# Optimization experiments

Measured on AMD Instinct MI355X. Metric: run time of the kernel, lower is better.

## Reference

```python
import jax, jax.numpy as jnp
from jax import lax
import numpy as np

DN = ('NHWC', 'HWIO', 'NHWC')


def extract_patches(x, k, stride):
    # tf.image.extract_patches with sizes [1,k,k,1], strides [1,s,s,1], SAME padding.
    # Output depth ordering matches TF: (ki, kj, channel).
    B, H, W, C = x.shape
    oh = -(-H // stride)
    ow = -(-W // stride)
    ph = max((oh - 1) * stride + k - H, 0)
    pw = max((ow - 1) * stride + k - W, 0)
    xp = jnp.pad(x, ((0, 0), (ph // 2, ph - ph // 2), (pw // 2, pw - pw // 2), (0, 0)))
    cols = [xp[:, i:i + stride * (oh - 1) + 1:stride, j:j + stride * (ow - 1) + 1:stride, :]
            for i in range(k) for j in range(k)]
    return jnp.stack(cols, axis=3).reshape(B, oh, ow, k * k * C)


def contextual_attention(x, mask_s, rate=2, fuse_k=3, softmax_scale=10.0):
    B, H, W, C = x.shape
    k = rate * 2 - 1  # 3
    # raw (full-resolution) patches used as deconv filters: [B,k,k,C,L]
    raw = extract_patches(x, k, rate)
    h, w = raw.shape[1], raw.shape[2]
    L = h * w
    raw_f = raw.reshape(B, L, k, k, C).transpose(0, 2, 3, 4, 1)
    # downsample src/ref by rate (extract_patches with size 1 == strided slice)
    src = x[:, ::rate, ::rate, :]  # [B,h,w,C]
    feats = extract_patches(src, k, 1).reshape(B, L, k, k, C).transpose(0, 2, 3, 4, 1)  # [B,k,k,C,L]
    # NOTE: source normalizes by sum of squares over axes (0,1,2) = (batch,kh,kw) -> [C,L], no sqrt
    denom = jnp.maximum(jnp.sum(feats * feats, axis=(0, 1, 2)), 1e-8)
    ref_feat = feats / denom
    # mask: maxpool 16/16 then 3/1, then invert
    m = lax.reduce_window(mask_s, -jnp.inf, lax.max, (1, 16, 16, 1), (1, 16, 16, 1), 'SAME')
    m = lax.reduce_window(m, -jnp.inf, lax.max, (1, 3, 3, 1), (1, 1, 1, 1), 'SAME')
    mm = 1.0 - m  # [B,h,w,1]
    # per-sample correlation: conv src_b with its own normalized patch bank
    corr = lambda s, f: lax.conv_general_dilated(s[None], f, (1, 1), 'SAME', dimension_numbers=DN)[0]
    y = jax.vmap(corr)(src, ref_feat)  # [B,h,w,L]
    # fuse: diagonal (identity) 3x3 convs over the (query, key) score plane, both orderings
    fuse_w = jnp.eye(fuse_k, dtype=x.dtype).reshape(fuse_k, fuse_k, 1, 1)
    yi = y.reshape(B, h * w, L, 1)
    yi = lax.conv_general_dilated(yi, fuse_w, (1, 1), 'SAME', dimension_numbers=DN)
    yi = yi.reshape(B, h, w, h, w).transpose(0, 2, 1, 4, 3).reshape(B, h * w, L, 1)
    yi = lax.conv_general_dilated(yi, fuse_w, (1, 1), 'SAME', dimension_numbers=DN)
    y = yi.reshape(B, w, h, w, h).transpose(0, 2, 1, 4, 3).reshape(B, h, w, L)
    # masked softmax over reference patches
    y = jax.nn.softmax(y * mm * softmax_scale, axis=-1) * mm
    # per-sample transposed conv (paste raw patches), matching tf.nn.conv2d_transpose SAME stride=rate
    pt = max((h - 1) * rate + k - H, 0)
    pl = max((w - 1) * rate + k - W, 0)
    pad_h = (k - 1 - pt // 2, k - 1 - (pt - pt // 2))
    pad_w = (k - 1 - pl // 2, k - 1 - (pl - pl // 2))

    def deconv(y_b, f_b):
        wg = jnp.flip(f_b, axis=(0, 1)).swapaxes(2, 3)  # [k,k,L,C]
        return lax.conv_general_dilated(y_b[None], wg, (1, 1), (pad_h, pad_w),
                                        lhs_dilation=(rate, rate), dimension_numbers=DN)[0]

    y_up = jax.vmap(deconv)(y, raw_f)  # [B,H,W,C]
    return y_up, y


def gated_conv(x, w, b, dw, pw, db):
    # gen_conv_gated_ds: Conv2D -> ELU gated by SeparableConv2D -> channel softmax
    x1 = jax.nn.elu(lax.conv_general_dilated(x, w, (1, 1), 'SAME', dimension_numbers=DN) + b)
    x2 = lax.conv_general_dilated(x, dw, (1, 1), 'SAME', feature_group_count=x.shape[-1],
                                  dimension_numbers=DN)
    x2 = lax.conv_general_dilated(x2, pw, (1, 1), 'SAME', dimension_numbers=DN) + db
    return x1 * jax.nn.softmax(x2, axis=-1)


def setup_inputs():
    key = jax.random.key(0)
    ks = jax.random.split(key, 8)
    B, H, W, C, dim = 8, 64, 64, 128, 128
    s = 0.05
    x = jax.random.normal(ks[0], (B, H, W, C), jnp.float32)
    mask_s = jnp.zeros((B, 16 * H // 2, 16 * W // 2, 1), jnp.float32)
    mask_s = mask_s.at[:, 128:384, 128:384, :].set(1.0)
    return {
        'x': x,
        'mask_s': mask_s,
        'w1': jax.random.normal(ks[1], (3, 3, C, dim), jnp.float32) * s,
        'b1': jnp.zeros((dim,), jnp.float32),
        'dw1': jax.random.normal(ks[2], (3, 3, 1, C), jnp.float32) * s,
        'pw1': jax.random.normal(ks[3], (1, 1, C, dim), jnp.float32) * s,
        'db1': jnp.zeros((dim,), jnp.float32),
        'w2': jax.random.normal(ks[4], (3, 3, dim + C, dim), jnp.float32) * s,
        'b2': jnp.zeros((dim,), jnp.float32),
        'dw2': jax.random.normal(ks[5], (3, 3, 1, dim + C), jnp.float32) * s,
        'pw2': jax.random.normal(ks[6], (1, 1, dim + C, dim), jnp.float32) * s,
        'db2': jnp.zeros((dim,), jnp.float32),
    }


def reference(x, mask_s, w1, b1, dw1, pw1, db1, w2, b2, dw2, pw2, db2):
    y_up, corres = contextual_attention(x, mask_s)
    a = gated_conv(y_up, w1, b1, dw1, pw1, db1)
    a = jnp.concatenate([a, x], axis=3)
    a = gated_conv(a, w2, b2, dw2, pw2, db2)
    return a, corres
```

## Files before the change

### kernel.cpp

```cpp
#include <hip/hip_runtime.h>
#include <hip/hip_bf16.h>


#define BOFF_SP      0
#define BOFF_INVD    4734976
#define BOFF_SP16    5259264
#define BOFF_BF16    7626752
#define BOFF_T       0
#define BOFF_BP16    0
#define BOFF_YP16    18874368
#define BOFF_YUP     37748736
#define BOFF_SM      0
#define BOFF_P316    16777216
#define BOFF_A1      25698304
#define BOFF_X16     42475520
#define BOFF_WT1     69238784
#define BOFF_WT2     69828608
#define BOFF_PW1     71008256
#define BOFF_PW2     71041024
#define BOFF_M0      71106560
#define BOFF_MM      71139328

typedef float f32x4 __attribute__((ext_vector_type(4)));
typedef _Float16 f16x8 __attribute__((ext_vector_type(8)));

__global__ __launch_bounds__(256) void k_mask_pool(const float* __restrict__ mask, float* __restrict__ m0) {
    int blk = blockIdx.x;
    int b = blk >> 10, pq = blk & 1023, p = pq >> 5, q = pq & 31;
    int t = threadIdx.x, dy = t >> 4, dx = t & 15;
    float v = mask[((size_t)(b * 512 + p * 16 + dy)) * 512 + q * 16 + dx];
#pragma unroll
    for (int o = 32; o; o >>= 1) v = fmaxf(v, __shfl_xor(v, o));
    __shared__ float s[4];
    if ((t & 63) == 0) s[t >> 6] = v;
    __syncthreads();
    if (t == 0) m0[blk] = fmaxf(fmaxf(s[0], s[1]), fmaxf(s[2], s[3]));
}

__global__ void k_mask_dilate(const float* __restrict__ m0, float* __restrict__ mm) {
    int idx = blockIdx.x * 256 + threadIdx.x;
    if (idx >= 8192) return;
    int b = idx >> 10, pq = idx & 1023, p = pq >> 5, q = pq & 31;
    float v = -1e30f;
    for (int di = -1; di <= 1; ++di)
        for (int dj = -1; dj <= 1; ++dj) {
            int pp = p + di, qq = q + dj;
            if (pp >= 0 && pp < 32 && qq >= 0 && qq < 32)
                v = fmaxf(v, m0[(b << 10) + pp * 32 + qq]);
        }
    mm[idx] = 1.0f - v;
}

__global__ void k_srcpad(const float* __restrict__ x, float* __restrict__ sp) {
    int idx = blockIdx.x * 256 + threadIdx.x;
    if (idx >= 8 * 34 * 34 * 128) return;
    int c = idx & 127;
    int r = idx >> 7;
    int xx = r % 34; r /= 34;
    int yy = r % 34; int b = r / 34;
    float v = 0.f;
    if (yy >= 1 && yy <= 32 && xx >= 1 && xx <= 32)
        v = x[(((size_t)(b * 64 + (yy - 1) * 2)) * 64 + (xx - 1) * 2) * 128 + c];
    sp[idx] = v;
}

__global__ void k_sp16(const float* __restrict__ sp, _Float16* __restrict__ o) {
    int idx = blockIdx.x * 256 + threadIdx.x;
    if (idx >= 147968) return;
    const float* s = sp + (size_t)idx * 8;
    float4 v0 = *reinterpret_cast<const float4*>(s);
    float4 v1 = *reinterpret_cast<const float4*>(s + 4);
    f16x8 h;
    h[0] = (_Float16)v0.x; h[1] = (_Float16)v0.y; h[2] = (_Float16)v0.z; h[3] = (_Float16)v0.w;
    h[4] = (_Float16)v1.x; h[5] = (_Float16)v1.y; h[6] = (_Float16)v1.z; h[7] = (_Float16)v1.w;
    *reinterpret_cast<f16x8*>(o + (size_t)idx * 8) = h;
}

__global__ void k_invd(const float* __restrict__ sp, float* __restrict__ invd) {
    int idx = blockIdx.x * 256 + threadIdx.x;
    if (idx >= 1024 * 128) return;
    int c = idx & 127, l = idx >> 7, lh = l >> 5, lw = l & 31;
    float s = 0.f;
    for (int b = 0; b < 8; ++b)
#pragma unroll
        for (int i = 0; i < 3; ++i)
#pragma unroll
            for (int j = 0; j < 3; ++j) {
                float v = sp[(((size_t)(b * 34 + lh + i)) * 34 + (lw + j)) * 128 + c];
                s += v * v;
            }
    invd[idx] = 1.0f / fmaxf(s, 1e-8f);
}

__global__ void k_corr_B16(const float* __restrict__ sp, const float* __restrict__ invd,
                           _Float16* __restrict__ bf) {
    int idx = blockIdx.x * 256 + threadIdx.x;
    if (idx >= 1179648) return;
    int c8 = idx & 15; int rest = idx >> 4;
    int ij = rest % 9; int rest2 = rest / 9;
    int l = rest2 & 1023, b = rest2 >> 10;
    int lh = l >> 5, lw = l & 31;
    int i = (ij >= 6) ? 2 : (ij >= 3 ? 1 : 0);
    int j = ij - 3 * i;
    int c0 = c8 * 8;
    const float* s = sp + (((size_t)(b * 34 + lh + i)) * 34 + (lw + j)) * 128 + c0;
    const float* dv = invd + l * 128 + c0;
    f16x8 h;
#pragma unroll
    for (int u = 0; u < 8; ++u) h[u] = (_Float16)(s[u] * dv[u]);
    size_t off = ((size_t)(b * 1024 + l)) * 1152 + ij * 128 + c0;
    *reinterpret_cast<f16x8*>(bf + off) = h;
}

__global__ void k_deconv_B16(const float* __restrict__ x, _Float16* __restrict__ bp) {
    int idx = blockIdx.x * 256 + threadIdx.x;
    if (idx >= 1179648) return;
    int l8 = idx & 127; int rest = idx >> 7;
    int c = rest & 127; int rest2 = rest >> 7;
    int ij = rest2 % 9; int b = rest2 / 9;
    int ip = (ij >= 6) ? 2 : (ij >= 3 ? 1 : 0);
    int jp = ij - 3 * ip;
    int l0 = l8 * 8;
    int lh = l0 >> 5, lw0 = l0 & 31;
    int rr = 2 * lh + ip;
    f16x8 h;
#pragma unroll
    for (int u = 0; u < 8; ++u) {
        int ss = 2 * (lw0 + u) + jp;
        float v = (rr < 64 && ss < 64) ? x[(((size_t)(b * 64 + rr)) * 64 + ss) * 128 + c] : 0.f;
        h[u] = (_Float16)v;
    }
    size_t off = (((size_t)(b * 9 + ij)) * 128 + c) * 1024 + l0;
    *reinterpret_cast<f16x8*>(bp + off) = h;
}

__global__ __launch_bounds__(512) void k_corr_mfma(const _Float16* __restrict__ sp16,
                                                   const _Float16* __restrict__ bf,
                                                   float* __restrict__ outy) {
    const int bid = blockIdx.x;
    const int xcd = bid & 7, slot = bid >> 3;
    const int tm = slot & 7, pg = slot >> 3;
    const int panel = pg * 8 + xcd;
    const int b = panel >> 4, tn = panel & 15;
    __shared__ _Float16 Aa[128][40];
    __shared__ _Float16 Ab[128][40];
    const int tid = threadIdx.x;
    const int w = tid >> 6, lane = tid & 63, m = lane & 15, g = lane >> 4;
    const int rh = w & 1, cg = w >> 1;
    f32x4 acc[4];
#pragma unroll
    for (int mf = 0; mf < 4; ++mf) acc[mf] = f32x4{0.f, 0.f, 0.f, 0.f};
    const int srow = tid >> 2, scc = (tid & 3) * 8;
    const int pq = tm * 128 + srow, p = pq >> 5, q = pq & 31;
    const int col0 = tn * 64 + cg * 16 + m;
    const size_t boff = ((size_t)b * 1024 + col0) * 1152 + g * 8;

    auto aoff = [&](int kt) -> size_t {
        int ij = kt >> 7;
        int i = (ij >= 6) ? 2 : (ij >= 3 ? 1 : 0);
        int j = ij - 3 * i;
        int c0 = (kt & 127) + scc;
        return (((size_t)(b * 34 + p + i)) * 34 + (q + j)) * 128 + c0;
    };
    f16x8 ara = *reinterpret_cast<const f16x8*>(sp16 + aoff(0));
    f16x8 arb = *reinterpret_cast<const f16x8*>(sp16 + aoff(32));
    f16x8 nba = *reinterpret_cast<const f16x8*>(bf + boff);
    f16x8 nbb = *reinterpret_cast<const f16x8*>(bf + boff + 32);

    for (int kt = 0; kt < 1152; kt += 64) {
        __syncthreads();
        *reinterpret_cast<f16x8*>(&Aa[srow][scc]) = ara;
        *reinterpret_cast<f16x8*>(&Ab[srow][scc]) = arb;
        __syncthreads();
        const int ktn = (kt + 64 < 1152) ? kt + 64 : kt;
        f16x8 cba = nba, cbb = nbb;
        ara = *reinterpret_cast<const f16x8*>(sp16 + aoff(ktn));
        arb = *reinterpret_cast<const f16x8*>(sp16 + aoff(ktn + 32));
        nba = *reinterpret_cast<const f16x8*>(bf + boff + ktn);
        nbb = *reinterpret_cast<const f16x8*>(bf + boff + ktn + 32);

        f16x8 av;
#pragma unroll
        for (int mf = 0; mf < 4; ++mf) {
            av = *reinterpret_cast<const f16x8*>(&Aa[rh * 64 + mf * 16 + m][g * 8]);
            acc[mf] = __builtin_amdgcn_mfma_f32_16x16x32_f16(av, cba, acc[mf], 0, 0, 0);
            av = *reinterpret_cast<const f16x8*>(&Ab[rh * 64 + mf * 16 + m][g * 8]);
            acc[mf] = __builtin_amdgcn_mfma_f32_16x16x32_f16(av, cbb, acc[mf], 0, 0, 0);
        }
    }
#pragma unroll
    for (int mf = 0; mf < 4; ++mf) {
        int row = tm * 128 + rh * 64 + mf * 16 + g * 4;
#pragma unroll
        for (int r = 0; r < 4; ++r)
            outy[((size_t)b << 20) + (size_t)(row + r) * 1024 + col0] = acc[mf][r];
    }
}

__global__ __launch_bounds__(512) void k_deconv_mfma(const _Float16* __restrict__ yp16,
                                                     const _Float16* __restrict__ bp,
                                                     float* __restrict__ yup) {
    const int bid = blockIdx.x;
    const int xcd = bid & 7, slot = bid >> 3;
    const int tm = slot & 7, pg = slot >> 3;
    const int panel = pg * 8 + xcd;
    const int b = panel / 9, tn = panel % 9;
    __shared__ _Float16 Aa[128][40];
    __shared__ _Float16 Ab[128][40];
    const int tid = threadIdx.x;
    const int w = tid >> 6, lane = tid & 63, m = lane & 15, g = lane >> 4;
    const int rh = w & 1, cg = w >> 1;
    f32x4 acc[4][2];
#pragma unroll
    for (int mf = 0; mf < 4; ++mf)
#pragma unroll
        for (int nn = 0; nn < 2; ++nn) acc[mf][nn] = f32x4{0.f, 0.f, 0.f, 0.f};
    const int srow = tid >> 2, scc = (tid & 3) * 8;
    const int c0 = cg * 32 + m;
    const _Float16* abase = yp16 + ((size_t)b << 20) + (size_t)(tm * 128 + srow) * 1024 + scc;
    const size_t boff0 = (((size_t)(b * 9 + tn)) * 128 + c0) * 1024 + g * 8;
    const size_t boff1 = (((size_t)(b * 9 + tn)) * 128 + c0 + 16) * 1024 + g * 8;

    f16x8 ara = *reinterpret_cast<const f16x8*>(abase);
    f16x8 arb = *reinterpret_cast<const f16x8*>(abase + 32);
    f16x8 nb0a = *reinterpret_cast<const f16x8*>(bp + boff0);
    f16x8 nb0b = *reinterpret_cast<const f16x8*>(bp + boff0 + 32);
    f16x8 nb1a = *reinterpret_cast<const f16x8*>(bp + boff1);
    f16x8 nb1b = *reinterpret_cast<const f16x8*>(bp + boff1 + 32);

    for (int kt = 0; kt < 1024; kt += 64) {
        __syncthreads();
        *reinterpret_cast<f16x8*>(&Aa[srow][scc]) = ara;
        *reinterpret_cast<f16x8*>(&Ab[srow][scc]) = arb;
        __syncthreads();
        const int ktn = (kt + 64 < 1024) ? kt + 64 : kt;
        f16x8 cb0a = nb0a, cb0b = nb0b, cb1a = nb1a, cb1b = nb1b;
        ara = *reinterpret_cast<const f16x8*>(abase + ktn);
        arb = *reinterpret_cast<const f16x8*>(abase + ktn + 32);
        nb0a = *reinterpret_cast<const f16x8*>(bp + boff0 + ktn);
        nb0b = *reinterpret_cast<const f16x8*>(bp + boff0 + ktn + 32);
        nb1a = *reinterpret_cast<const f16x8*>(bp + boff1 + ktn);
        nb1b = *reinterpret_cast<const f16x8*>(bp + boff1 + ktn + 32);

        f16x8 av;
#pragma unroll
        for (int mf = 0; mf < 4; ++mf) {
            av = *reinterpret_cast<const f16x8*>(&Aa[rh * 64 + mf * 16 + m][g * 8]);
            acc[mf][0] = __builtin_amdgcn_mfma_f32_16x16x32_f16(av, cb0a, acc[mf][0], 0, 0, 0);
            acc[mf][1] = __builtin_amdgcn_mfma_f32_16x16x32_f16(av, cb1a, acc[mf][1], 0, 0, 0);
            av = *reinterpret_cast<const f16x8*>(&Ab[rh * 64 + mf * 16 + m][g * 8]);
            acc[mf][0] = __builtin_amdgcn_mfma_f32_16x16x32_f16(av, cb0b, acc[mf][0], 0, 0, 0);
            acc[mf][1] = __builtin_amdgcn_mfma_f32_16x16x32_f16(av, cb1b, acc[mf][1], 0, 0, 0);
        }
    }
    const int ip = (tn >= 6) ? 2 : (tn >= 3 ? 1 : 0);
    const int jp = tn - 3 * ip;
#pragma unroll
    for (int mf = 0; mf < 4; ++mf) {
        int uvb = tm * 128 + rh * 64 + mf * 16 + g * 4;
#pragma unroll
        for (int nn = 0; nn < 2; ++nn) {
            int c = c0 + nn * 16;
#pragma unroll
            for (int r = 0; r < 4; ++r) {
                int uv = uvb + r;
                int uu = uv >> 5, vv = uv & 31;
                int P = 2 * uu + ip, Q = 2 * vv + jp;
                if (P < 64 && Q < 64)
                    atomicAdd(&yup[(((size_t)(b * 64 + P)) * 64 + Q) * 128 + c], acc[mf][nn][r]);
            }
        }
    }
}

__global__ void k_fuse1(const float* __restrict__ in, float* __restrict__ out) {
    size_t idx = (size_t)blockIdx.x * 256 + threadIdx.x;
    if (idx >= (size_t)8 * 1024 * 1024) return;
    int t = (int)(idx & 1023);
    int s = (int)((idx >> 10) & 1023);
    int b = (int)(idx >> 20);
    const float* base = in + ((size_t)b << 20);
    float v = base[(size_t)s * 1024 + t];
    if (s > 0 && t > 0) v += base[(size_t)(s - 1) * 1024 + (t - 1)];
    if (s < 1023 && t < 1023) v += base[(size_t)(s + 1) * 1024 + (t + 1)];
    out[idx] = v;
}

__global__ void k_fuse2(const float* __restrict__ in, float* __restrict__ out) {
    size_t idx = (size_t)blockIdx.x * 256 + threadIdx.x;
    if (idx >= (size_t)8 * 1024 * 1024) return;
    int t = (int)(idx & 1023);
    int s = (int)((idx >> 10) & 1023);
    int b = (int)(idx >> 20);
    int m0 = ((s & 31) << 5) + (s >> 5);
    int n0 = ((t & 31) << 5) + (t >> 5);
    const float* base = in + ((size_t)b << 20);
    float v = 0.f;
#pragma unroll
    for (int d = -1; d <= 1; ++d) {
        int m = m0 + d, n = n0 + d;
        if (m >= 0 && m < 1024 && n >= 0 && n < 1024)
            v += base[(size_t)(((m & 31) << 5) + (m >> 5)) * 1024 + (((n & 31) << 5) + (n >> 5))];
    }
    out[idx] = v;
}

__global__ __launch_bounds__(256) void k_softmax1024(const float* __restrict__ yv,
                                                     const float* __restrict__ mm,
                                                     float* __restrict__ outc,
                                                     _Float16* __restrict__ yp16) {
    int row = blockIdx.x;
    const float* base = yv + (size_t)row * 1024;
    float mmv = mm[row];
    int t = threadIdx.x;
    float vals[4];
    float mx = -1e30f;
#pragma unroll
    for (int i = 0; i < 4; ++i) {
        vals[i] = base[t + i * 256] * mmv * 10.0f;
        mx = fmaxf(mx, vals[i]);
    }
#pragma unroll
    for (int o = 32; o; o >>= 1) mx = fmaxf(mx, __shfl_xor(mx, o));
    __shared__ float red[8];
    if ((t & 63) == 0) red[t >> 6] = mx;
    __syncthreads();
    mx = fmaxf(fmaxf(red[0], red[1]), fmaxf(red[2], red[3]));
    float s = 0.f;
#pragma unroll
    for (int i = 0; i < 4; ++i) {
        vals[i] = expf(vals[i] - mx);
        s += vals[i];
    }
#pragma unroll
    for (int o = 32; o; o >>= 1) s += __shfl_xor(s, o);
    if ((t & 63) == 0) red[4 + (t >> 6)] = s;
    __syncthreads();
    s = red[4] + red[5] + red[6] + red[7];
    float inv = mmv / s;
#pragma unroll
    for (int i = 0; i < 4; ++i) {
        float pv = vals[i] * inv;
        outc[(size_t)row * 1024 + t + i * 256] = pv;
        yp16[(size_t)row * 1024 + t + i * 256] = (_Float16)pv;
    }
}

__global__ __launch_bounds__(256) void k_pad16(const float* __restrict__ in,
                                               _Float16* __restrict__ o) {
    int idx = blockIdx.x * 256 + threadIdx.x;
    int c8 = idx & 15;
    int r = idx >> 4;
    int pc = r % 66; r /= 66;
    int pr = r % 66; int b = r / 66;
    f16x8 h;
    if (pr >= 1 && pr <= 64 && pc >= 1 && pc <= 64) {
        const float* s = in + (((size_t)(b * 64 + pr - 1)) * 64 + (pc - 1)) * 128 + c8 * 8;
        float4 v0 = *reinterpret_cast<const float4*>(s);
        float4 v1 = *reinterpret_cast<const float4*>(s + 4);
        h[0] = (_Float16)v0.x; h[1] = (_Float16)v0.y; h[2] = (_Float16)v0.z; h[3] = (_Float16)v0.w;
        h[4] = (_Float16)v1.x; h[5] = (_Float16)v1.y; h[6] = (_Float16)v1.z; h[7] = (_Float16)v1.w;
    } else {
#pragma unroll
        for (int u = 0; u < 8; ++u) h[u] = (_Float16)0.f;
    }
    *reinterpret_cast<f16x8*>(o + (size_t)idx * 8) = h;
}

__global__ void k_wt16(const float* __restrict__ w, _Float16* __restrict__ o, int CI) {
    int idx = blockIdx.x * 256 + threadIdx.x;
    if (idx >= 9 * CI * 128) return;
    int ci = idx % CI; int rest = idx / CI;
    int co = rest & 127; int ij = rest >> 7;
    o[idx] = (_Float16)w[((size_t)ij * CI + ci) * 128 + co];
}

__global__ void k_pw16(const float* __restrict__ pw, _Float16* __restrict__ out, int CI) {
    int idx = blockIdx.x * 256 + threadIdx.x;
    if (idx >= CI * 128) return;
    int co = idx & 127, ci = idx >> 7;
    out[(size_t)co * CI + ci] = (_Float16)pw[idx];
}

template <int CI>
__global__ __launch_bounds__(256, 2) void k_dwpw_mfma(const _Float16* __restrict__ in0,
                                                      const _Float16* __restrict__ in1,
                                                      const float* __restrict__ dwW,
                                                      const _Float16* __restrict__ pwt,
                                                      const float* __restrict__ db,
                                                      float* __restrict__ smout) {
    const int bid = blockIdx.x;
    const int swz = (bid & 7) * 64 + (bid >> 3);
    const int b = swz >> 6, P = swz & 63;
    const int t = threadIdx.x;
    const int w = t >> 6, lane = t & 63, m = lane & 15, g = lane >> 4;
    __shared__ _Float16 Adw[64 * CI];
    __shared__ float red[2][4][64];
    char* ab = (char*)Adw;
    const int px = lane;
    const int cb = w * (CI / 4);
    float dwacc[CI / 4];
#pragma unroll
    for (int u = 0; u < CI / 4; ++u) dwacc[u] = 0.f;
#pragma unroll
    for (int i = 0; i < 3; ++i) {
#pragma unroll
        for (int j = 0; j < 3; ++j) {
            const int ij = i * 3 + j;
#pragma unroll
            for (int c8 = 0; c8 < CI / 32; ++c8) {
                const int c = cb + c8 * 8;
                const _Float16* ph = (CI == 256 && c >= 128) ? in1 : in0;
                const int cc = (CI == 256 && c >= 128) ? (c - 128) : c;
                size_t off = (((size_t)b * 66 + P + i) * 66 + px + j) * 128 + cc;
                f16x8 vh = *reinterpret_cast<const f16x8*>(ph + off);
#pragma unroll
                for (int u = 0; u < 8; ++u)
                    dwacc[c8 * 8 + u] = fmaf((float)vh[u], dwW[ij * CI + c + u], dwacc[c8 * 8 + u]);
            }
        }
    }
#pragma unroll
    for (int c8 = 0; c8 < CI / 32; ++c8) {
        f16x8 hv;
#pragma unroll
        for (int u = 0; u < 8; ++u) hv[u] = (_Float16)dwacc[c8 * 8 + u];
        int byte = px * (CI * 2) + (cb + c8 * 8) * 2;
        int sz = byte ^ ((px & 7) << 4);
        *reinterpret_cast<f16x8*>(ab + sz) = hv;
    }
    __syncthreads();
    f32x4 acc[4][2];
#pragma unroll
    for (int mt = 0; mt < 4; ++mt)
#pragma unroll
        for (int nn = 0; nn < 2; ++nn) acc[mt][nn] = f32x4{0.f, 0.f, 0.f, 0.f};
    const int co0 = w * 32 + m;
#pragma unroll
    for (int kc = 0; kc < CI / 32; ++kc) {
        f16x8 av[4];
#pragma unroll
        for (int mt = 0; mt < 4; ++mt) {
            int prow = mt * 16 + m;
            int byte = prow * (CI * 2) + (kc * 32 + g * 8) * 2;
            int sz = byte ^ ((prow & 7) << 4);
            av[mt] = *reinterpret_cast<const f16x8*>(ab + sz);
        }
#pragma unroll
        for (int nn = 0; nn < 2; ++nn) {
            f16x8 bv = *reinterpret_cast<const f16x8*>(pwt + (size_t)(co0 + nn * 16) * CI + kc * 32 + g * 8);
#pragma unroll
            for (int mt = 0; mt < 4; ++mt)
                acc[mt][nn] = __builtin_amdgcn_mfma_f32_16x16x32_f16(av[mt], bv, acc[mt][nn], 0, 0, 0);
        }
    }
    float db0 = db[co0], db1 = db[co0 + 16];
    float mx[4][4];
#pragma unroll
    for (int mt = 0; mt < 4; ++mt)
#pragma unroll
        for (int r = 0; r < 4; ++r) {
            acc[mt][0][r] += db0;
            acc[mt][1][r] += db1;
            float v = fmaxf(acc[mt][0][r], acc[mt][1][r]);
#pragma unroll
            for (int o = 1; o <= 8; o <<= 1) v = fmaxf(v, __shfl_xor(v, o));
            mx[mt][r] = v;
        }
    if (m == 0) {
#pragma unroll
        for (int mt = 0; mt < 4; ++mt)
#pragma unroll
            for (int r = 0; r < 4; ++r) red[0][w][mt * 16 + g * 4 + r] = mx[mt][r];
    }
    __syncthreads();
    float sume[4][4];
#pragma unroll
    for (int mt = 0; mt < 4; ++mt)
#pragma unroll
        for (int r = 0; r < 4; ++r) {
            int p = mt * 16 + g * 4 + r;
            float M = fmaxf(fmaxf(red[0][0][p], red[0][1][p]), fmaxf(red[0][2][p], red[0][3][p]));
            acc[mt][0][r] = expf(acc[mt][0][r] - M);
            acc[mt][1][r] = expf(acc[mt][1][r] - M);
            float s = acc[mt][0][r] + acc[mt][1][r];
#pragma unroll
            for (int o = 1; o <= 8; o <<= 1) s += __shfl_xor(s, o);
            sume[mt][r] = s;
        }
    if (m == 0) {
#pragma unroll
        for (int mt = 0; mt < 4; ++mt)
#pragma unroll
            for (int r = 0; r < 4; ++r) red[1][w][mt * 16 + g * 4 + r] = sume[mt][r];
    }
    __syncthreads();
#pragma unroll
    for (int mt = 0; mt < 4; ++mt)
#pragma unroll
        for (int r = 0; r < 4; ++r) {
            int p = mt * 16 + g * 4 + r;
            float S = red[1][0][p] + red[1][1][p] + red[1][2][p] + red[1][3][p];
            float inv = 1.0f / S;
            size_t pix = ((size_t)b * 64 + P) * 64 + p;
            smout[pix * 128 + co0] = acc[mt][0][r] * inv;
            smout[pix * 128 + co0 + 16] = acc[mt][1][r] * inv;
        }
}

template <int CI>
__global__ __launch_bounds__(256, 4) void k_conv_lds(const _Float16* __restrict__ in0,
                                                     const _Float16* __restrict__ in1,
                                                     const _Float16* __restrict__ wt,
                                                     const float* __restrict__ bias,
                                                     const float* __restrict__ sm,
                                                     float* __restrict__ out) {
    const int bid = blockIdx.x;
    const int idx = (bid & 7) * 128 + (bid >> 3);
    const int row = idx >> 1, cohalf = idx & 1;
    const int b = row >> 6, P = row & 63;
    const int tid = threadIdx.x;
    const int w = tid >> 6, lane = tid & 63;
    const int m = lane & 15, g = lane >> 4;
    __shared__ _Float16 S[66 * 128];
    char* sb = (char*)S;
    f32x4 acc[4];
#pragma unroll
    for (int mt = 0; mt < 4; ++mt) acc[mt] = f32x4{0.f, 0.f, 0.f, 0.f};
    const int cow = cohalf * 64 + w * 16 + m;

#pragma unroll
    for (int half = 0; half < CI / 128; ++half) {
        const _Float16* ih = (half == 0) ? in0 : in1;
        const size_t rbase0 = ((size_t)b * 66 + P) * 66 * 128;
#pragma unroll
        for (int i = 0; i < 3; ++i) {
            __syncthreads();
            const size_t rsrc = rbase0 + (size_t)i * 66 * 128;
#pragma unroll
            for (int e0 = 0; e0 < 1056; e0 += 256) {
                int e = e0 + tid;
                if (e < 1056) {
                    int px = e >> 4, c8 = e & 15;
                    int lin = px * 256 + c8 * 16;
                    int sz = lin ^ ((px & 7) << 4);
                    size_t so = rsrc + (size_t)px * 128 + c8 * 8;
                    *reinterpret_cast<f16x8*>(sb + sz) = *reinterpret_cast<const f16x8*>(ih + so);
                }
            }
            __syncthreads();
#pragma unroll
            for (int j = 0; j < 3; ++j) {
                const int ij = i * 3 + j;
                const _Float16* wp = wt + ((size_t)ij * 128 + cow) * CI + half * 128 + g * 8;
#pragma unroll
                for (int ci0 = 0; ci0 < 128; ci0 += 32) {
                    f16x8 bv = *reinterpret_cast<const f16x8*>(wp + ci0);
                    f16x8 av[4];
#pragma unroll
                    for (int mt = 0; mt < 4; ++mt) {
                        int px = mt * 16 + m + j;
                        int lin = px * 256 + ci0 * 2 + g * 16;
                        int sz = lin ^ ((px & 7) << 4);
                        av[mt] = *reinterpret_cast<const f16x8*>(sb + sz);
                    }
#pragma unroll
                    for (int mt = 0; mt < 4; ++mt)
                        acc[mt] = __builtin_amdgcn_mfma_f32_16x16x32_f16(av[mt], bv, acc[mt], 0, 0, 0);
                }
            }
        }
    }
    const float bb = bias[cow];
#pragma unroll
    for (int mt = 0; mt < 4; ++mt) {
#pragma unroll
        for (int r = 0; r < 4; ++r) {
            int Q = mt * 16 + g * 4 + r;
            size_t pix = ((size_t)b * 64 + P) * 64 + Q;
            float z = acc[mt][r] + bb;
            z = z > 0.f ? z : expm1f(z);
            out[pix * 128 + cow] = z * sm[pix * 128 + cow];
        }
    }
}

extern "C" void kernel_launch(void* const* d_in, const int* in_sizes, int n_in,
                              void* d_out, int out_size, void* d_ws, size_t ws_size,
                              hipStream_t stream) {
    const float* x    = (const float*)d_in[0];
    const float* mask = (const float*)d_in[1];
    const float* w1   = (const float*)d_in[2];
    const float* b1   = (const float*)d_in[3];
    const float* dw1  = (const float*)d_in[4];
    const float* pw1  = (const float*)d_in[5];
    const float* db1  = (const float*)d_in[6];
    const float* w2   = (const float*)d_in[7];
    const float* b2   = (const float*)d_in[8];
    const float* dw2  = (const float*)d_in[9];
    const float* pw2  = (const float*)d_in[10];
    const float* db2  = (const float*)d_in[11];

    float* out_a = (float*)d_out;
    float* out_c = out_a + 4194304;

    char* wsb = (char*)d_ws;
    float* sp      = (float*)(wsb + BOFF_SP);
    float* invd    = (float*)(wsb + BOFF_INVD);
    _Float16* sp16 = (_Float16*)(wsb + BOFF_SP16);
    _Float16* bf16b = (_Float16*)(wsb + BOFF_BF16);
    float* Tbuf    = (float*)(wsb + BOFF_T);
    _Float16* bp16 = (_Float16*)(wsb + BOFF_BP16);
    _Float16* yp16 = (_Float16*)(wsb + BOFF_YP16);
    float* yup     = (float*)(wsb + BOFF_YUP);
    float* smb     = (float*)(wsb + BOFF_SM);
    _Float16* p316 = (_Float16*)(wsb + BOFF_P316);
    float* a1      = (float*)(wsb + BOFF_A1);
    _Float16* x16  = (_Float16*)(wsb + BOFF_X16);
    _Float16* wt1  = (_Float16*)(wsb + BOFF_WT1);
    _Float16* wt2  = (_Float16*)(wsb + BOFF_WT2);
    _Float16* pw1t = (_Float16*)(wsb + BOFF_PW1);
    _Float16* pw2t = (_Float16*)(wsb + BOFF_PW2);
    float* m0      = (float*)(wsb + BOFF_M0);
    float* mmb     = (float*)(wsb + BOFF_MM);

    k_mask_pool<<<8192, 256, 0, stream>>>(mask, m0);
    k_mask_dilate<<<32, 256, 0, stream>>>(m0, mmb);
    k_srcpad<<<4624, 256, 0, stream>>>(x, sp);
    k_sp16<<<579, 256, 0, stream>>>(sp, sp16);
    k_invd<<<512, 256, 0, stream>>>(sp, invd);
    k_wt16<<<576, 256, 0, stream>>>(w1, wt1, 128);
    k_wt16<<<1152, 256, 0, stream>>>(w2, wt2, 256);
    k_pw16<<<64, 256, 0, stream>>>(pw1, pw1t, 128);
    k_pw16<<<128, 256, 0, stream>>>(pw2, pw2t, 256);
    k_corr_B16<<<4608, 256, 0, stream>>>(sp, invd, bf16b);
    k_corr_mfma<<<1024, 512, 0, stream>>>(sp16, bf16b, out_c);
    k_fuse1<<<32768, 256, 0, stream>>>(out_c, Tbuf);
    k_fuse2<<<32768, 256, 0, stream>>>(Tbuf, out_c);
    k_deconv_B16<<<4608, 256, 0, stream>>>(x, bp16);
    k_softmax1024<<<8192, 256, 0, stream>>>(out_c, mmb, out_c, yp16);
    hipMemsetAsync(yup, 0, (size_t)4194304 * sizeof(float), stream);
    k_deconv_mfma<<<576, 512, 0, stream>>>(yp16, bp16, yup);
    k_pad16<<<2178, 256, 0, stream>>>(yup, p316);
    k_pad16<<<2178, 256, 0, stream>>>(x, x16);
    k_dwpw_mfma<128><<<512, 256, 0, stream>>>(p316, nullptr, dw1, pw1t, db1, smb);
    k_conv_lds<128><<<1024, 256, 0, stream>>>(p316, nullptr, wt1, b1, smb, a1);
    k_pad16<<<2178, 256, 0, stream>>>(a1, p316);
    k_dwpw_mfma<256><<<512, 256, 0, stream>>>(p316, x16, dw2, pw2t, db2, smb);
    k_conv_lds<256><<<1024, 256, 0, stream>>>(p316, x16, wt2, b2, smb, out_a);
}
```

Before: 436.4 us.

## Deepen global prefetch to two stages in MFMA GEMMs and fuse fp16 source cast

The correlation and deconvolution MFMA kernels now prefetch global A and B fragments two K-tiles ahead instead of one, rotating register queues, to hide more load latency. Separately, the fp16 copy of the padded source is written directly by the padding kernel, which removes one small launch and a re-read of the fp32 buffer. The deeper prefetch raises register pressure, which may lower occupancy.

```diff
diff --git a/kernel.cpp b/kernel.cpp
--- a/kernel.cpp
+++ b/kernel.cpp
@@ -51,7 +51,8 @@
     mm[idx] = 1.0f - v;
 }
 
-__global__ void k_srcpad(const float* __restrict__ x, float* __restrict__ sp) {
+__global__ void k_srcpad(const float* __restrict__ x, float* __restrict__ sp,
+                         _Float16* __restrict__ sp16) {
     int idx = blockIdx.x * 256 + threadIdx.x;
     if (idx >= 8 * 34 * 34 * 128) return;
     int c = idx & 127;
@@ -62,18 +63,7 @@
     if (yy >= 1 && yy <= 32 && xx >= 1 && xx <= 32)
         v = x[(((size_t)(b * 64 + (yy - 1) * 2)) * 64 + (xx - 1) * 2) * 128 + c];
     sp[idx] = v;
-}
-
-__global__ void k_sp16(const float* __restrict__ sp, _Float16* __restrict__ o) {
-    int idx = blockIdx.x * 256 + threadIdx.x;
-    if (idx >= 147968) return;
-    const float* s = sp + (size_t)idx * 8;
-    float4 v0 = *reinterpret_cast<const float4*>(s);
-    float4 v1 = *reinterpret_cast<const float4*>(s + 4);
-    f16x8 h;
-    h[0] = (_Float16)v0.x; h[1] = (_Float16)v0.y; h[2] = (_Float16)v0.z; h[3] = (_Float16)v0.w;
-    h[4] = (_Float16)v1.x; h[5] = (_Float16)v1.y; h[6] = (_Float16)v1.z; h[7] = (_Float16)v1.w;
-    *reinterpret_cast<f16x8*>(o + (size_t)idx * 8) = h;
+    sp16[idx] = (_Float16)v;
 }
 
 __global__ void k_invd(const float* __restrict__ sp, float* __restrict__ invd) {
@@ -162,22 +152,28 @@
         int c0 = (kt & 127) + scc;
         return (((size_t)(b * 34 + p + i)) * 34 + (q + j)) * 128 + c0;
     };
-    f16x8 ara = *reinterpret_cast<const f16x8*>(sp16 + aoff(0));
-    f16x8 arb = *reinterpret_cast<const f16x8*>(sp16 + aoff(32));
-    f16x8 nba = *reinterpret_cast<const f16x8*>(bf + boff);
-    f16x8 nbb = *reinterpret_cast<const f16x8*>(bf + boff + 32);
+    f16x8 aq_a = *reinterpret_cast<const f16x8*>(sp16 + aoff(0));
+    f16x8 aq_b = *reinterpret_cast<const f16x8*>(sp16 + aoff(32));
+    f16x8 aq2_a = *reinterpret_cast<const f16x8*>(sp16 + aoff(64));
+    f16x8 aq2_b = *reinterpret_cast<const f16x8*>(sp16 + aoff(96));
+    f16x8 bq_a = *reinterpret_cast<const f16x8*>(bf + boff);
+    f16x8 bq_b = *reinterpret_cast<const f16x8*>(bf + boff + 32);
+    f16x8 bq2_a = *reinterpret_cast<const f16x8*>(bf + boff + 64);
+    f16x8 bq2_b = *reinterpret_cast<const f16x8*>(bf + boff + 96);
 
     for (int kt = 0; kt < 1152; kt += 64) {
         __syncthreads();
-        *reinterpret_cast<f16x8*>(&Aa[srow][scc]) = ara;
-        *reinterpret_cast<f16x8*>(&Ab[srow][scc]) = arb;
+        *reinterpret_cast<f16x8*>(&Aa[srow][scc]) = aq_a;
+        *reinterpret_cast<f16x8*>(&Ab[srow][scc]) = aq_b;
         __syncthreads();
-        const int ktn = (kt + 64 < 1152) ? kt + 64 : kt;
-        f16x8 cba = nba, cbb = nbb;
-        ara = *reinterpret_cast<const f16x8*>(sp16 + aoff(ktn));
-        arb = *reinterpret_cast<const f16x8*>(sp16 + aoff(ktn + 32));
-        nba = *reinterpret_cast<const f16x8*>(bf + boff + ktn);
-        nbb = *reinterpret_cast<const f16x8*>(bf + boff + ktn + 32);
+        const int kt2 = (kt + 128 < 1152) ? kt + 128 : kt;
+        f16x8 cba = bq_a, cbb = bq_b;
+        aq_a = aq2_a; aq_b = aq2_b;
+        aq2_a = *reinterpret_cast<const f16x8*>(sp16 + aoff(kt2));
+        aq2_b = *reinterpret_cast<const f16x8*>(sp16 + aoff(kt2 + 32));
+        bq_a = bq2_a; bq_b = bq2_b;
+        bq2_a = *reinterpret_cast<const f16x8*>(bf + boff + kt2);
+        bq2_b = *reinterpret_cast<const f16x8*>(bf + boff + kt2 + 32);
 
         f16x8 av;
 #pragma unroll
@@ -221,26 +217,35 @@
     const size_t boff0 = (((size_t)(b * 9 + tn)) * 128 + c0) * 1024 + g * 8;
     const size_t boff1 = (((size_t)(b * 9 + tn)) * 128 + c0 + 16) * 1024 + g * 8;
 
-    f16x8 ara = *reinterpret_cast<const f16x8*>(abase);
-    f16x8 arb = *reinterpret_cast<const f16x8*>(abase + 32);
-    f16x8 nb0a = *reinterpret_cast<const f16x8*>(bp + boff0);
-    f16x8 nb0b = *reinterpret_cast<const f16x8*>(bp + boff0 + 32);
-    f16x8 nb1a = *reinterpret_cast<const f16x8*>(bp + boff1);
-    f16x8 nb1b = *reinterpret_cast<const f16x8*>(bp + boff1 + 32);
+    f16x8 aq_a = *reinterpret_cast<const f16x8*>(abase);
+    f16x8 aq_b = *reinterpret_cast<const f16x8*>(abase + 32);
+    f16x8 aq2_a = *reinterpret_cast<const f16x8*>(abase + 64);
+    f16x8 aq2_b = *reinterpret_cast<const f16x8*>(abase + 96);
+    f16x8 b0q_a = *reinterpret_cast<const f16x8*>(bp + boff0);
+    f16x8 b0q_b = *reinterpret_cast<const f16x8*>(bp + boff0 + 32);
+    f16x8 b1q_a = *reinterpret_cast<const f16x8*>(bp + boff1);
+    f16x8 b1q_b = *reinterpret_cast<const f16x8*>(bp + boff1 + 32);
+    f16x8 b0q2_a = *reinterpret_cast<const f16x8*>(bp + boff0 + 64);
+    f16x8 b0q2_b = *reinterpret_cast<const f16x8*>(bp + boff0 + 96);
+    f16x8 b1q2_a = *reinterpret_cast<const f16x8*>(bp + boff1 + 64);
+    f16x8 b1q2_b = *reinterpret_cast<const f16x8*>(bp + boff1 + 96);
 
     for (int kt = 0; kt < 1024; kt += 64) {
         __syncthreads();
-        *reinterpret_cast<f16x8*>(&Aa[srow][scc]) = ara;
-        *reinterpret_cast<f16x8*>(&Ab[srow][scc]) = arb;
+        *reinterpret_cast<f16x8*>(&Aa[srow][scc]) = aq_a;
+        *reinterpret_cast<f16x8*>(&Ab[srow][scc]) = aq_b;
         __syncthreads();
-        const int ktn = (kt + 64 < 1024) ? kt + 64 : kt;
-        f16x8 cb0a = nb0a, cb0b = nb0b, cb1a = nb1a, cb1b = nb1b;
-        ara = *reinterpret_cast<const f16x8*>(abase + ktn);
-        arb = *reinterpret_cast<const f16x8*>(abase + ktn + 32);
-        nb0a = *reinterpret_cast<const f16x8*>(bp + boff0 + ktn);
-        nb0b = *reinterpret_cast<const f16x8*>(bp + boff0 + ktn + 32);
-        nb1a = *reinterpret_cast<const f16x8*>(bp + boff1 + ktn);
-        nb1b = *reinterpret_cast<const f16x8*>(bp + boff1 + ktn + 32);
+        const int kt2 = (kt + 128 < 1024) ? kt + 128 : kt;
+        f16x8 cb0a = b0q_a, cb0b = b0q_b, cb1a = b1q_a, cb1b = b1q_b;
+        aq_a = aq2_a; aq_b = aq2_b;
+        aq2_a = *reinterpret_cast<const f16x8*>(abase + kt2);
+        aq2_b = *reinterpret_cast<const f16x8*>(abase + kt2 + 32);
+        b0q_a = b0q2_a; b0q_b = b0q2_b;
+        b1q_a = b1q2_a; b1q_b = b1q2_b;
+        b0q2_a = *reinterpret_cast<const f16x8*>(bp + boff0 + kt2);
+        b0q2_b = *reinterpret_cast<const f16x8*>(bp + boff0 + kt2 + 32);
+        b1q2_a = *reinterpret_cast<const f16x8*>(bp + boff1 + kt2);
+        b1q2_b = *reinterpret_cast<const f16x8*>(bp + boff1 + kt2 + 32);
 
         f16x8 av;
 #pragma unroll
@@ -626,8 +631,7 @@
 
     k_mask_pool<<<8192, 256, 0, stream>>>(mask, m0);
     k_mask_dilate<<<32, 256, 0, stream>>>(m0, mmb);
-    k_srcpad<<<4624, 256, 0, stream>>>(x, sp);
-    k_sp16<<<579, 256, 0, stream>>>(sp, sp16);
+    k_srcpad<<<4624, 256, 0, stream>>>(x, sp, sp16);
     k_invd<<<512, 256, 0, stream>>>(sp, invd);
     k_wt16<<<576, 256, 0, stream>>>(w1, wt1, 128);
     k_wt16<<<1152, 256, 0, stream>>>(w2, wt2, 256);
```

New measurement: 431.9 us. No clear change (-1.0%).
